# Performance work log

Hardware: AMD Instinct MI355X
Metric: run time of the kernel (lower is better)

The kernel has to match this reference:

```python
import jax, jax.numpy as jnp
import numpy as np

N = 50000
E = 800000
IN_F, HID, OUT_F = 512, 256, 64
BN_EPS = 1e-5


def setup_inputs() -> dict:
    key = jax.random.key(0)
    ks = jax.random.split(key, 8)
    x = jax.random.normal(ks[0], (N, IN_F), dtype=jnp.float32)
    edge_rows = jax.random.randint(ks[1], (E,), 0, N, dtype=jnp.int32)
    edge_cols = jax.random.randint(ks[2], (E,), 0, N, dtype=jnp.int32)
    edge_vals = jax.random.uniform(ks[3], (E,), dtype=jnp.float32)
    # xavier_uniform for weights, zeros for biases (as in the torch module)
    lim1 = float(np.sqrt(6.0 / (IN_F + HID)))
    lim2 = float(np.sqrt(6.0 / (HID + OUT_F)))
    W1 = jax.random.uniform(ks[4], (IN_F, HID), minval=-lim1, maxval=lim1, dtype=jnp.float32)
    b1 = jnp.zeros((HID,), dtype=jnp.float32)
    W2 = jax.random.uniform(ks[5], (HID, OUT_F), minval=-lim2, maxval=lim2, dtype=jnp.float32)
    b2 = jnp.zeros((OUT_F,), dtype=jnp.float32)
    # BatchNorm affine params (torch defaults: weight=1, bias=0)
    gamma1 = jnp.ones((HID,), dtype=jnp.float32)
    beta1 = jnp.zeros((HID,), dtype=jnp.float32)
    gamma2 = jnp.ones((OUT_F,), dtype=jnp.float32)
    beta2 = jnp.zeros((OUT_F,), dtype=jnp.float32)
    return dict(x=x, edge_rows=edge_rows, edge_cols=edge_cols, edge_vals=edge_vals,
                W1=W1, b1=b1, gamma1=gamma1, beta1=beta1,
                W2=W2, b2=b2, gamma2=gamma2, beta2=beta2)


def _spmm(rows, cols, vals, dense):
    # sparse [N,N] @ dense [N,F] via gather + segment-sum scatter
    msgs = vals[:, None] * dense[cols]            # [E, F]
    return jax.ops.segment_sum(msgs, rows, num_segments=N)


def _batchnorm(h, gamma, beta):
    # training-mode BatchNorm1d: batch statistics over nodes (biased var)
    mean = jnp.mean(h, axis=0)
    var = jnp.var(h, axis=0)
    return gamma * (h - mean) * jax.lax.rsqrt(var + BN_EPS) + beta


def reference(x, edge_rows, edge_cols, edge_vals,
              W1, b1, gamma1, beta1, W2, b2, gamma2, beta2):
    # layer 1: GCN conv -> BN -> ReLU (dropout is identity in eval / reference)
    h = _spmm(edge_rows, edge_cols, edge_vals, x @ W1) + b1
    h = jax.nn.relu(_batchnorm(h, gamma1, beta1))
    # layer 2: GCN conv -> BN -> log_softmax over classes
    h = _spmm(edge_rows, edge_cols, edge_vals, h @ W2) + b2
    h = _batchnorm(h, gamma2, beta2)
    return jax.nn.log_softmax(h, axis=1)
```

## Files before the change

### kernel.cpp

```cpp
#include <hip/hip_runtime.h>

typedef __attribute__((ext_vector_type(8))) short short8;
typedef __attribute__((ext_vector_type(4))) float f32x4;
typedef __attribute__((ext_vector_type(8))) unsigned short ushort8;

__device__ __forceinline__ unsigned short f2bf(float f) {
  unsigned int u = __builtin_bit_cast(unsigned int, f);
  u += 0x7fffu + ((u >> 16) & 1u);
  return (unsigned short)(u >> 16);
}
__device__ __forceinline__ float bf2f(unsigned short b) {
  return __builtin_bit_cast(float, ((unsigned int)b) << 16);
}
__device__ __forceinline__ void gload_lds16(const void* g, void* l) {
  __builtin_amdgcn_global_load_lds(
      (const __attribute__((address_space(1))) void*)g,
      (__attribute__((address_space(3))) void*)l, 16, 0, 0);
}

__global__ __launch_bounds__(256) void cvt_w1t(
    const float* __restrict__ W1, unsigned short* __restrict__ W1T)
{
  int idx = blockIdx.x * 256 + threadIdx.x;
  int n = idx >> 9, k = idx & 511;
  W1T[idx] = f2bf(W1[(size_t)k * 256 + n]);
}

__global__ __launch_bounds__(256) void cvt_w2t(
    const float* __restrict__ W2, unsigned short* __restrict__ W2T)
{
  int idx = blockIdx.x * 256 + threadIdx.x;
  int n = idx >> 8, k = idx & 255;
  W2T[idx] = f2bf(W2[(size_t)k * 64 + n]);
}

__global__ __launch_bounds__(256) void gemm1_mfma(
    const float* __restrict__ x,
    const unsigned short* __restrict__ w1t,
    unsigned short* __restrict__ H1,
    int M)
{
  __shared__ unsigned short As[64 * 64];
  __shared__ unsigned short Bs[256 * 64];
  const int tid = threadIdx.x;
  const int wid = tid >> 6, lane = tid & 63;
  const int wc = wid;
  const int m0 = blockIdx.x * 64;

  const int srow = tid >> 3;
  const int ls = ((tid & 7) ^ (srow & 7)) * 8;
  const unsigned short* gB = &w1t[(size_t)srow * 512 + ls];
  char* lB = (char*)Bs + (size_t)wid * 1024;

  f32x4 acc[4][4] = {};

  for (int kt = 0; kt < 8; ++kt) {
    const int k0 = kt * 64;
#pragma unroll
    for (int i = 0; i < 8; ++i)
      gload_lds16(gB + (size_t)i * 32 * 512 + k0, lB + (size_t)i * 4096);
#pragma unroll
    for (int i = 0; i < 2; ++i) {
      int chunk = tid + 256 * i;
      int r = chunk >> 3, c = chunk & 7;
      int grow = m0 + r;
      float v[8] = {0.f, 0.f, 0.f, 0.f, 0.f, 0.f, 0.f, 0.f};
      if (grow < M) {
        float4 lo = *(const float4*)&x[(size_t)grow * 512 + k0 + c * 8];
        float4 hi = *(const float4*)&x[(size_t)grow * 512 + k0 + c * 8 + 4];
        v[0] = lo.x; v[1] = lo.y; v[2] = lo.z; v[3] = lo.w;
        v[4] = hi.x; v[5] = hi.y; v[6] = hi.z; v[7] = hi.w;
      }
      ushort8 o;
#pragma unroll
      for (int j = 0; j < 8; ++j) o[j] = f2bf(v[j]);
      *(ushort8*)((char*)As + r * 128 + ((c ^ (r & 7)) * 16)) = o;
    }
    __syncthreads();

#pragma unroll
    for (int kk = 0; kk < 2; ++kk) {
      short8 a[4], b[4];
#pragma unroll
      for (int m = 0; m < 4; ++m) {
        int row = m * 16 + (lane & 15);
        int phys = (kk * 4 + (lane >> 4)) ^ (row & 7);
        a[m] = *(const short8*)((const char*)As + row * 128 + phys * 16);
      }
#pragma unroll
      for (int n = 0; n < 4; ++n) {
        int col = wc * 64 + n * 16 + (lane & 15);
        int phys = (kk * 4 + (lane >> 4)) ^ (col & 7);
        b[n] = *(const short8*)((const char*)Bs + col * 128 + phys * 16);
      }
#pragma unroll
      for (int m = 0; m < 4; ++m)
#pragma unroll
        for (int n = 0; n < 4; ++n)
          acc[m][n] = __builtin_amdgcn_mfma_f32_16x16x32_bf16(a[m], b[n], acc[m][n], 0, 0, 0);
    }
    __syncthreads();
  }

  const int colbase = wc * 64 + (lane & 15);
#pragma unroll
  for (int m = 0; m < 4; ++m) {
    int rowbase = m0 + m * 16 + (lane >> 4) * 4;
#pragma unroll
    for (int j = 0; j < 4; ++j) {
      int row = rowbase + j;
      if (row < M) {
#pragma unroll
        for (int n = 0; n < 4; ++n)
          H1[(size_t)row * 256 + colbase + n * 16] = f2bf(acc[m][n][j]);
      }
    }
  }
}

__global__ __launch_bounds__(256) void gemm2_mfma(
    const unsigned short* __restrict__ A,
    const unsigned short* __restrict__ w2t,
    const float* __restrict__ scsh,
    unsigned short* __restrict__ H2,
    int M)
{
  __shared__ unsigned short As[128 * 64];
  __shared__ unsigned short Bs[64 * 64];
  const int tid = threadIdx.x;
  const int wid = tid >> 6, lane = tid & 63;
  const int wr = wid >> 1, wc = wid & 1;
  const int m0 = blockIdx.x * 128;

  const int srow = tid >> 3;
  const int ls = ((tid & 7) ^ (srow & 7)) * 8;
  const unsigned short* gB = &w2t[(size_t)srow * 256 + ls];
  char* lB = (char*)Bs + (size_t)wid * 1024;

  f32x4 acc[4][2] = {};

  for (int kt = 0; kt < 4; ++kt) {
    const int k0 = kt * 64;
#pragma unroll
    for (int i = 0; i < 2; ++i)
      gload_lds16(gB + (size_t)i * 32 * 256 + k0, lB + (size_t)i * 4096);
#pragma unroll
    for (int i = 0; i < 4; ++i) {
      int chunk = tid + 256 * i;
      int r = chunk >> 3, c = chunk & 7;
      int gk = k0 + c * 8;
      ushort8 u = *(const ushort8*)&A[(size_t)(m0 + r) * 256 + gk];
      float4 sc0 = *(const float4*)&scsh[gk];
      float4 sc1 = *(const float4*)&scsh[gk + 4];
      float4 sh0 = *(const float4*)&scsh[256 + gk];
      float4 sh1 = *(const float4*)&scsh[256 + gk + 4];
      ushort8 o;
      o[0] = f2bf(fmaxf(bf2f(u[0]) * sc0.x + sh0.x, 0.f));
      o[1] = f2bf(fmaxf(bf2f(u[1]) * sc0.y + sh0.y, 0.f));
      o[2] = f2bf(fmaxf(bf2f(u[2]) * sc0.z + sh0.z, 0.f));
      o[3] = f2bf(fmaxf(bf2f(u[3]) * sc0.w + sh0.w, 0.f));
      o[4] = f2bf(fmaxf(bf2f(u[4]) * sc1.x + sh1.x, 0.f));
      o[5] = f2bf(fmaxf(bf2f(u[5]) * sc1.y + sh1.y, 0.f));
      o[6] = f2bf(fmaxf(bf2f(u[6]) * sc1.z + sh1.z, 0.f));
      o[7] = f2bf(fmaxf(bf2f(u[7]) * sc1.w + sh1.w, 0.f));
      *(ushort8*)((char*)As + r * 128 + ((c ^ (r & 7)) * 16)) = o;
    }
    __syncthreads();

#pragma unroll
    for (int kk = 0; kk < 2; ++kk) {
      short8 a[4], b[2];
#pragma unroll
      for (int m = 0; m < 4; ++m) {
        int row = wr * 64 + m * 16 + (lane & 15);
        int phys = (kk * 4 + (lane >> 4)) ^ (row & 7);
        a[m] = *(const short8*)((const char*)As + row * 128 + phys * 16);
      }
#pragma unroll
      for (int n = 0; n < 2; ++n) {
        int col = wc * 32 + n * 16 + (lane & 15);
        int phys = (kk * 4 + (lane >> 4)) ^ (col & 7);
        b[n] = *(const short8*)((const char*)Bs + col * 128 + phys * 16);
      }
#pragma unroll
      for (int m = 0; m < 4; ++m)
#pragma unroll
        for (int n = 0; n < 2; ++n)
          acc[m][n] = __builtin_amdgcn_mfma_f32_16x16x32_bf16(a[m], b[n], acc[m][n], 0, 0, 0);
    }
    __syncthreads();
  }

  const int colbase = wc * 32 + (lane & 15);
#pragma unroll
  for (int m = 0; m < 4; ++m) {
    int rowbase = m0 + wr * 64 + m * 16 + (lane >> 4) * 4;
#pragma unroll
    for (int j = 0; j < 4; ++j) {
      int row = rowbase + j;
      if (row < M) {
#pragma unroll
        for (int n = 0; n < 2; ++n)
          H2[(size_t)row * 64 + colbase + n * 16] = f2bf(acc[m][n][j]);
      }
    }
  }
}

__global__ __launch_bounds__(256) void edge_hist(
    const int* __restrict__ rows, int* __restrict__ cnt, int E)
{
  int e = blockIdx.x * 256 + threadIdx.x;
  if (e < E) atomicAdd(&cnt[rows[e]], 1);
}

__global__ __launch_bounds__(256) void scan_blocksum(
    const int* __restrict__ cnt, int* __restrict__ bsum, int Nrows)
{
  int i = blockIdx.x * 256 + threadIdx.x;
  int v = (i < Nrows) ? cnt[i] : 0;
#pragma unroll
  for (int off = 1; off < 64; off <<= 1) v += __shfl_xor(v, off);
  __shared__ int wsum[4];
  if ((threadIdx.x & 63) == 0) wsum[threadIdx.x >> 6] = v;
  __syncthreads();
  if (threadIdx.x == 0)
    bsum[blockIdx.x] = wsum[0] + wsum[1] + wsum[2] + wsum[3];
}

__global__ __launch_bounds__(256) void scan_boff(
    const int* __restrict__ bsum, int* __restrict__ boff, int NB)
{
  __shared__ int lds[256];
  int t = threadIdx.x;
  int v = (t < NB) ? bsum[t] : 0;
  lds[t] = v;
  __syncthreads();
  for (int off = 1; off < 256; off <<= 1) {
    int u = (t >= off) ? lds[t - off] : 0;
    __syncthreads();
    lds[t] += u;
    __syncthreads();
  }
  boff[t] = (t == 0) ? 0 : lds[t - 1];
}

__global__ __launch_bounds__(256) void scan_write(
    const int* __restrict__ cnt, const int* __restrict__ boff,
    int* __restrict__ rowptr, int* __restrict__ cursor, int Nrows, int E)
{
  __shared__ int lds[256];
  int t = threadIdx.x;
  int i = blockIdx.x * 256 + t;
  int v = (i < Nrows) ? cnt[i] : 0;
  lds[t] = v;
  __syncthreads();
  for (int off = 1; off < 256; off <<= 1) {
    int u = (t >= off) ? lds[t - off] : 0;
    __syncthreads();
    lds[t] += u;
    __syncthreads();
  }
  int excl = boff[blockIdx.x] + lds[t] - v;
  if (i < Nrows) { rowptr[i] = excl; cursor[i] = excl; }
  if (i == Nrows) rowptr[i] = E;
}

__global__ __launch_bounds__(256) void edge_scatter(
    const int* __restrict__ rows, const int* __restrict__ cols,
    const float* __restrict__ vals, int* __restrict__ cursor,
    int* __restrict__ scols, float* __restrict__ svals, int E)
{
  int e = blockIdx.x * 256 + threadIdx.x;
  if (e < E) {
    int r = rows[e];
    int p = atomicAdd(&cursor[r], 1);
    scols[p] = cols[e];
    svals[p] = vals[e];
  }
}

__global__ __launch_bounds__(256) void spmm_gather_bf(
    const int* __restrict__ rowptr, const int* __restrict__ scols,
    const float* __restrict__ svals, const unsigned short* __restrict__ D,
    unsigned short* __restrict__ out, int Nrows)
{
  const int lane = threadIdx.x & 63;
  const int r = blockIdx.x * 4 + (threadIdx.x >> 6);
  if (r >= Nrows) return;
  const int s = rowptr[r], e = rowptr[r + 1];
  float4 acc = make_float4(0.f, 0.f, 0.f, 0.f);
  int j = s;
  for (; j + 1 < e; j += 2) {
    int c0 = scols[j], c1 = scols[j + 1];
    float v0 = svals[j], v1 = svals[j + 1];
    ushort4 d0 = *(const ushort4*)&D[(size_t)c0 * 256 + lane * 4];
    ushort4 d1 = *(const ushort4*)&D[(size_t)c1 * 256 + lane * 4];
    acc.x = fmaf(v0, bf2f(d0.x), acc.x); acc.y = fmaf(v0, bf2f(d0.y), acc.y);
    acc.z = fmaf(v0, bf2f(d0.z), acc.z); acc.w = fmaf(v0, bf2f(d0.w), acc.w);
    acc.x = fmaf(v1, bf2f(d1.x), acc.x); acc.y = fmaf(v1, bf2f(d1.y), acc.y);
    acc.z = fmaf(v1, bf2f(d1.z), acc.z); acc.w = fmaf(v1, bf2f(d1.w), acc.w);
  }
  if (j < e) {
    int c = scols[j]; float v = svals[j];
    ushort4 d = *(const ushort4*)&D[(size_t)c * 256 + lane * 4];
    acc.x = fmaf(v, bf2f(d.x), acc.x); acc.y = fmaf(v, bf2f(d.y), acc.y);
    acc.z = fmaf(v, bf2f(d.z), acc.z); acc.w = fmaf(v, bf2f(d.w), acc.w);
  }
  ushort4 ov;
  ov.x = f2bf(acc.x); ov.y = f2bf(acc.y); ov.z = f2bf(acc.z); ov.w = f2bf(acc.w);
  *(ushort4*)&out[(size_t)r * 256 + lane * 4] = ov;
}

__global__ __launch_bounds__(256) void spmm_gather_bf64(
    const int* __restrict__ rowptr, const int* __restrict__ scols,
    const float* __restrict__ svals, const unsigned short* __restrict__ D,
    float* __restrict__ out, int Nrows)
{
  const int lane = threadIdx.x & 63;
  const int r = blockIdx.x * 4 + (threadIdx.x >> 6);
  if (r >= Nrows) return;
  const int s = rowptr[r], e = rowptr[r + 1];
  float acc = 0.f;
  int j = s;
  for (; j + 1 < e; j += 2) {
    int c0 = scols[j], c1 = scols[j + 1];
    float v0 = svals[j], v1 = svals[j + 1];
    acc = fmaf(v0, bf2f(D[(size_t)c0 * 64 + lane]), acc);
    acc = fmaf(v1, bf2f(D[(size_t)c1 * 64 + lane]), acc);
  }
  if (j < e) acc = fmaf(svals[j], bf2f(D[(size_t)scols[j] * 64 + lane]), acc);
  out[(size_t)r * 64 + lane] = acc;
}

__global__ __launch_bounds__(256) void bn_stats_bf256(
    const unsigned short* __restrict__ H, float* __restrict__ partials, int Nrows)
{
  const int cc = threadIdx.x & 31;
  const int c = cc * 8;
  const int rr = threadIdx.x >> 5;
  float s[8] = {}, q[8] = {};
  for (int r = blockIdx.x * 8 + rr; r < Nrows; r += gridDim.x * 8) {
    ushort8 u = *(const ushort8*)&H[(size_t)r * 256 + c];
#pragma unroll
    for (int j = 0; j < 8; ++j) {
      float f = bf2f(u[j]);
      s[j] += f; q[j] += f * f;
    }
  }
  __shared__ float lds[256][16];
  float* L = lds[threadIdx.x];
#pragma unroll
  for (int j = 0; j < 8; ++j) { L[j] = s[j]; L[8 + j] = q[j]; }
  __syncthreads();
  if (rr == 0) {
#pragma unroll
    for (int r2 = 1; r2 < 8; ++r2) {
      float* Mm = lds[cc + r2 * 32];
#pragma unroll
      for (int j = 0; j < 8; ++j) { s[j] += Mm[j]; q[j] += Mm[8 + j]; }
    }
    float* P = &partials[(size_t)blockIdx.x * 512];
#pragma unroll
    for (int j = 0; j < 8; ++j) { P[c + j] = s[j]; P[256 + c + j] = q[j]; }
  }
}

__global__ __launch_bounds__(256) void bn_stats64(
    const float* __restrict__ H, float* __restrict__ partials, int Nrows)
{
  const int cc = threadIdx.x % 16;
  const int c = cc * 4;
  const int rr = threadIdx.x / 16;
  float4 s = make_float4(0.f, 0.f, 0.f, 0.f);
  float4 q = make_float4(0.f, 0.f, 0.f, 0.f);
  for (int r = blockIdx.x * 16 + rr; r < Nrows; r += gridDim.x * 16) {
    float4 v = *(const float4*)&H[(size_t)r * 64 + c];
    s.x += v.x; s.y += v.y; s.z += v.z; s.w += v.w;
    q.x += v.x * v.x; q.y += v.y * v.y; q.z += v.z * v.z; q.w += v.w * v.w;
  }
  __shared__ float lds[256][8];
  float* L = lds[threadIdx.x];
  L[0] = s.x; L[1] = s.y; L[2] = s.z; L[3] = s.w;
  L[4] = q.x; L[5] = q.y; L[6] = q.z; L[7] = q.w;
  __syncthreads();
  if (rr == 0) {
#pragma unroll
    for (int r2 = 1; r2 < 16; ++r2) {
      float* Mm = lds[cc + r2 * 16];
      s.x += Mm[0]; s.y += Mm[1]; s.z += Mm[2]; s.w += Mm[3];
      q.x += Mm[4]; q.y += Mm[5]; q.z += Mm[6]; q.w += Mm[7];
    }
    float* P = &partials[(size_t)blockIdx.x * 128];
    *(float4*)&P[c] = s;
    *(float4*)&P[64 + c] = q;
  }
}

template<int C>
__global__ __launch_bounds__(256) void bn_finalize_par(
    const float* __restrict__ partials,
    const float* __restrict__ gamma, const float* __restrict__ beta,
    float* __restrict__ scsh, int G, float invN)
{
  const int c = blockIdx.x;
  const int t = threadIdx.x;
  float sum = 0.f, sq = 0.f;
  for (int g = t; g < G; g += 256) {
    sum += partials[(size_t)g * 2 * C + c];
    sq  += partials[(size_t)g * 2 * C + C + c];
  }
#pragma unroll
  for (int off = 1; off < 64; off <<= 1) {
    sum += __shfl_xor(sum, off);
    sq  += __shfl_xor(sq, off);
  }
  __shared__ float ws[4][2];
  if ((t & 63) == 0) { ws[t >> 6][0] = sum; ws[t >> 6][1] = sq; }
  __syncthreads();
  if (t == 0) {
    sum = ws[0][0] + ws[1][0] + ws[2][0] + ws[3][0];
    sq  = ws[0][1] + ws[1][1] + ws[2][1] + ws[3][1];
    float mean = sum * invN;
    float var = sq * invN - mean * mean;
    float rstd = rsqrtf(var + 1e-5f);
    float sc = gamma[c] * rstd;
    scsh[c] = sc;
    scsh[C + c] = beta[c] - mean * sc;
  }
}

__global__ __launch_bounds__(256) void bn_lsm(
    const float* __restrict__ H, const float* __restrict__ scsh,
    float* __restrict__ out, int Nrows)
{
  int lane = threadIdx.x & 63;
  int r = blockIdx.x * 4 + (threadIdx.x >> 6);
  if (r >= Nrows) return;
  float y = H[(size_t)r * 64 + lane] * scsh[lane] + scsh[64 + lane];
  float m = y;
#pragma unroll
  for (int off = 32; off >= 1; off >>= 1) m = fmaxf(m, __shfl_xor(m, off));
  float ex = expf(y - m);
  float s = ex;
#pragma unroll
  for (int off = 32; off >= 1; off >>= 1) s += __shfl_xor(s, off);
  out[(size_t)r * 64 + lane] = (y - m) - logf(s);
}

extern "C" void kernel_launch(void* const* d_in, const int* in_sizes, int n_in,
                              void* d_out, int out_size, void* d_ws, size_t ws_size,
                              hipStream_t stream) {
  const float* x      = (const float*)d_in[0];
  const int*   erow   = (const int*)  d_in[1];
  const int*   ecol   = (const int*)  d_in[2];
  const float* eval   = (const float*)d_in[3];
  const float* W1     = (const float*)d_in[4];
  const float* gamma1 = (const float*)d_in[6];
  const float* beta1  = (const float*)d_in[7];
  const float* W2     = (const float*)d_in[8];
  const float* gamma2 = (const float*)d_in[10];
  const float* beta2  = (const float*)d_in[11];

  const int N = in_sizes[0] / 512;
  const int E = in_sizes[1];

  char* ws = (char*)d_ws;
  unsigned short* H1b   = (unsigned short*)(ws + 0);
  float* partials1      = (float*)(ws + 0);
  unsigned short* H2b   = (unsigned short*)(ws + 0);
  float* H2AGG          = (float*)(ws + 12800000);
  unsigned short* H1AGGb= (unsigned short*)(ws + 51200000);
  float* partials2      = (float*)(ws + 51200000);
  unsigned short* w1t   = (unsigned short*)(ws + 76865536);
  float* scsh1          = (float*)(ws + 77127680);
  float* scsh2          = (float*)(ws + 77129728);
  int*   rowptr         = (int*)(ws + 77130240);
  int*   cnt            = (int*)(ws + 77330244);
  int*   cursor         = (int*)(ws + 77530244);
  int*   scols          = (int*)(ws + 77730244);
  float* svals          = (float*)(ws + 80930244);
  int*   bsum           = (int*)(ws + 84130244);
  int*   boff           = (int*)(ws + 84131268);
  unsigned short* w2t   = (unsigned short*)(ws + 84132352);

  hipMemsetAsync(cnt, 0, (size_t)N * 4, stream);

  const dim3 blk(256);
  const int eblocks = (E + 255) / 256;
  const int NB = (N + 255) / 256;

  edge_hist<<<eblocks, blk, 0, stream>>>(erow, cnt, E);
  scan_blocksum<<<NB, blk, 0, stream>>>(cnt, bsum, N);
  scan_boff<<<1, blk, 0, stream>>>(bsum, boff, NB);
  scan_write<<<NB + 1, blk, 0, stream>>>(cnt, boff, rowptr, cursor, N, E);
  edge_scatter<<<eblocks, blk, 0, stream>>>(erow, ecol, eval, cursor, scols, svals, E);

  cvt_w1t<<<512, blk, 0, stream>>>(W1, w1t);
  cvt_w2t<<<64, blk, 0, stream>>>(W2, w2t);

  gemm1_mfma<<<(N + 63) / 64, blk, 0, stream>>>(x, w1t, H1b, N);
  spmm_gather_bf<<<(N + 3) / 4, blk, 0, stream>>>(rowptr, scols, svals, H1b, H1AGGb, N);
  bn_stats_bf256<<<256, blk, 0, stream>>>(H1AGGb, partials1, N);
  bn_finalize_par<256><<<256, blk, 0, stream>>>(partials1, gamma1, beta1, scsh1, 256, 1.0f / N);
  gemm2_mfma<<<(N + 127) / 128, blk, 0, stream>>>(H1AGGb, w2t, scsh1, H2b, N);
  spmm_gather_bf64<<<(N + 3) / 4, blk, 0, stream>>>(rowptr, scols, svals, H2b, H2AGG, N);
  bn_stats64<<<256, blk, 0, stream>>>(H2AGG, partials2, N);
  bn_finalize_par<64><<<64, blk, 0, stream>>>(partials2, gamma2, beta2, scsh2, 256, 1.0f / N);
  bn_lsm<<<(N + 3) / 4, blk, 0, stream>>>(H2AGG, scsh2, (float*)d_out, N);
}
```

Measured before the change: 303.9 us.

## Double-buffer GEMM1 tiles, pack CSR col/val pairs, unroll SpMM gathers by four

GEMM1 now uses double-buffered LDS. The next K-tile of x is loaded into registers and W1 is staged into the alternate buffer while MFMAs run on the current tile, so global loads overlap compute. The CSR column indices and values are interleaved into one int2 array, so each edge takes one 8-byte load instead of two separate streams. Both SpMM gather kernels are unrolled by four with two accumulators to raise memory-level parallelism. The cost is twice the LDS in GEMM1, which may lower occupancy, plus a slightly different float summation order.

```diff
diff --git a/kernel.cpp b/kernel.cpp
--- a/kernel.cpp
+++ b/kernel.cpp
@@ -40,8 +40,8 @@
     unsigned short* __restrict__ H1,
     int M)
 {
-  __shared__ unsigned short As[64 * 64];
-  __shared__ unsigned short Bs[256 * 64];
+  __shared__ unsigned short As[2][64 * 64];
+  __shared__ unsigned short Bs[2][256 * 64];
   const int tid = threadIdx.x;
   const int wid = tid >> 6, lane = tid & 63;
   const int wc = wid;
@@ -50,34 +50,55 @@
   const int srow = tid >> 3;
   const int ls = ((tid & 7) ^ (srow & 7)) * 8;
   const unsigned short* gB = &w1t[(size_t)srow * 512 + ls];
-  char* lB = (char*)Bs + (size_t)wid * 1024;
-
-  f32x4 acc[4][4] = {};
-
-  for (int kt = 0; kt < 8; ++kt) {
-    const int k0 = kt * 64;
+
+  const int ar0 = tid >> 3;
+  const int ar1 = ar0 + 32;
+  const int ac  = tid & 7;
+  const int arow0 = m0 + ar0;
+  const int arow1 = m0 + ar1;
+
+  float4 a0lo, a0hi, a1lo, a1hi;
+
+  auto loadA = [&](int k0) {
+    a0lo = make_float4(0.f, 0.f, 0.f, 0.f); a0hi = a0lo; a1lo = a0lo; a1hi = a0lo;
+    if (arow0 < M) {
+      a0lo = *(const float4*)&x[(size_t)arow0 * 512 + k0 + ac * 8];
+      a0hi = *(const float4*)&x[(size_t)arow0 * 512 + k0 + ac * 8 + 4];
+    }
+    if (arow1 < M) {
+      a1lo = *(const float4*)&x[(size_t)arow1 * 512 + k0 + ac * 8];
+      a1hi = *(const float4*)&x[(size_t)arow1 * 512 + k0 + ac * 8 + 4];
+    }
+  };
+  auto writeA = [&](int buf) {
+    float v0[8] = {a0lo.x, a0lo.y, a0lo.z, a0lo.w, a0hi.x, a0hi.y, a0hi.z, a0hi.w};
+    float v1[8] = {a1lo.x, a1lo.y, a1lo.z, a1lo.w, a1hi.x, a1hi.y, a1hi.z, a1hi.w};
+    ushort8 o0, o1;
+#pragma unroll
+    for (int j = 0; j < 8; ++j) { o0[j] = f2bf(v0[j]); o1[j] = f2bf(v1[j]); }
+    *(ushort8*)((char*)As[buf] + ar0 * 128 + ((ac ^ (ar0 & 7)) * 16)) = o0;
+    *(ushort8*)((char*)As[buf] + ar1 * 128 + ((ac ^ (ar1 & 7)) * 16)) = o1;
+  };
+  auto stageB = [&](int k0, int buf) {
+    char* lB = (char*)Bs[buf] + (size_t)wid * 1024;
 #pragma unroll
     for (int i = 0; i < 8; ++i)
       gload_lds16(gB + (size_t)i * 32 * 512 + k0, lB + (size_t)i * 4096);
-#pragma unroll
-    for (int i = 0; i < 2; ++i) {
-      int chunk = tid + 256 * i;
-      int r = chunk >> 3, c = chunk & 7;
-      int grow = m0 + r;
-      float v[8] = {0.f, 0.f, 0.f, 0.f, 0.f, 0.f, 0.f, 0.f};
-      if (grow < M) {
-        float4 lo = *(const float4*)&x[(size_t)grow * 512 + k0 + c * 8];
-        float4 hi = *(const float4*)&x[(size_t)grow * 512 + k0 + c * 8 + 4];
-        v[0] = lo.x; v[1] = lo.y; v[2] = lo.z; v[3] = lo.w;
-        v[4] = hi.x; v[5] = hi.y; v[6] = hi.z; v[7] = hi.w;
-      }
-      ushort8 o;
-#pragma unroll
-      for (int j = 0; j < 8; ++j) o[j] = f2bf(v[j]);
-      *(ushort8*)((char*)As + r * 128 + ((c ^ (r & 7)) * 16)) = o;
-    }
-    __syncthreads();
-
+  };
+
+  f32x4 acc[4][4] = {};
+
+  loadA(0);
+  stageB(0, 0);
+  writeA(0);
+  __syncthreads();
+
+  for (int kt = 0; kt < 8; ++kt) {
+    const int cur = kt & 1, nxt = cur ^ 1;
+    if (kt < 7) {
+      loadA((kt + 1) * 64);
+      stageB((kt + 1) * 64, nxt);
+    }
 #pragma unroll
     for (int kk = 0; kk < 2; ++kk) {
       short8 a[4], b[4];
@@ -85,13 +106,13 @@
       for (int m = 0; m < 4; ++m) {
         int row = m * 16 + (lane & 15);
         int phys = (kk * 4 + (lane >> 4)) ^ (row & 7);
-        a[m] = *(const short8*)((const char*)As + row * 128 + phys * 16);
+        a[m] = *(const short8*)((const char*)As[cur] + row * 128 + phys * 16);
       }
 #pragma unroll
       for (int n = 0; n < 4; ++n) {
         int col = wc * 64 + n * 16 + (lane & 15);
         int phys = (kk * 4 + (lane >> 4)) ^ (col & 7);
-        b[n] = *(const short8*)((const char*)Bs + col * 128 + phys * 16);
+        b[n] = *(const short8*)((const char*)Bs[cur] + col * 128 + phys * 16);
       }
 #pragma unroll
       for (int m = 0; m < 4; ++m)
@@ -99,6 +120,7 @@
         for (int n = 0; n < 4; ++n)
           acc[m][n] = __builtin_amdgcn_mfma_f32_16x16x32_bf16(a[m], b[n], acc[m][n], 0, 0, 0);
     }
+    if (kt < 7) writeA(nxt);
     __syncthreads();
   }
 
@@ -269,68 +291,85 @@
 __global__ __launch_bounds__(256) void edge_scatter(
     const int* __restrict__ rows, const int* __restrict__ cols,
     const float* __restrict__ vals, int* __restrict__ cursor,
-    int* __restrict__ scols, float* __restrict__ svals, int E)
+    int2* __restrict__ spack, int E)
 {
   int e = blockIdx.x * 256 + threadIdx.x;
   if (e < E) {
     int r = rows[e];
     int p = atomicAdd(&cursor[r], 1);
-    scols[p] = cols[e];
-    svals[p] = vals[e];
+    spack[p] = make_int2(cols[e], __float_as_int(vals[e]));
   }
 }
 
 __global__ __launch_bounds__(256) void spmm_gather_bf(
-    const int* __restrict__ rowptr, const int* __restrict__ scols,
-    const float* __restrict__ svals, const unsigned short* __restrict__ D,
+    const int* __restrict__ rowptr, const int2* __restrict__ sp,
+    const unsigned short* __restrict__ D,
     unsigned short* __restrict__ out, int Nrows)
 {
   const int lane = threadIdx.x & 63;
   const int r = blockIdx.x * 4 + (threadIdx.x >> 6);
   if (r >= Nrows) return;
   const int s = rowptr[r], e = rowptr[r + 1];
-  float4 acc = make_float4(0.f, 0.f, 0.f, 0.f);
+  float4 acc0 = make_float4(0.f, 0.f, 0.f, 0.f);
+  float4 acc1 = make_float4(0.f, 0.f, 0.f, 0.f);
   int j = s;
-  for (; j + 1 < e; j += 2) {
-    int c0 = scols[j], c1 = scols[j + 1];
-    float v0 = svals[j], v1 = svals[j + 1];
-    ushort4 d0 = *(const ushort4*)&D[(size_t)c0 * 256 + lane * 4];
-    ushort4 d1 = *(const ushort4*)&D[(size_t)c1 * 256 + lane * 4];
-    acc.x = fmaf(v0, bf2f(d0.x), acc.x); acc.y = fmaf(v0, bf2f(d0.y), acc.y);
-    acc.z = fmaf(v0, bf2f(d0.z), acc.z); acc.w = fmaf(v0, bf2f(d0.w), acc.w);
-    acc.x = fmaf(v1, bf2f(d1.x), acc.x); acc.y = fmaf(v1, bf2f(d1.y), acc.y);
-    acc.z = fmaf(v1, bf2f(d1.z), acc.z); acc.w = fmaf(v1, bf2f(d1.w), acc.w);
-  }
-  if (j < e) {
-    int c = scols[j]; float v = svals[j];
-    ushort4 d = *(const ushort4*)&D[(size_t)c * 256 + lane * 4];
-    acc.x = fmaf(v, bf2f(d.x), acc.x); acc.y = fmaf(v, bf2f(d.y), acc.y);
-    acc.z = fmaf(v, bf2f(d.z), acc.z); acc.w = fmaf(v, bf2f(d.w), acc.w);
+  for (; j + 3 < e; j += 4) {
+    int2 p0 = sp[j], p1 = sp[j + 1], p2 = sp[j + 2], p3 = sp[j + 3];
+    ushort4 d0 = *(const ushort4*)&D[(size_t)p0.x * 256 + lane * 4];
+    ushort4 d1 = *(const ushort4*)&D[(size_t)p1.x * 256 + lane * 4];
+    ushort4 d2 = *(const ushort4*)&D[(size_t)p2.x * 256 + lane * 4];
+    ushort4 d3 = *(const ushort4*)&D[(size_t)p3.x * 256 + lane * 4];
+    float v0 = __int_as_float(p0.y), v1 = __int_as_float(p1.y);
+    float v2 = __int_as_float(p2.y), v3 = __int_as_float(p3.y);
+    acc0.x = fmaf(v0, bf2f(d0.x), acc0.x); acc0.y = fmaf(v0, bf2f(d0.y), acc0.y);
+    acc0.z = fmaf(v0, bf2f(d0.z), acc0.z); acc0.w = fmaf(v0, bf2f(d0.w), acc0.w);
+    acc1.x = fmaf(v1, bf2f(d1.x), acc1.x); acc1.y = fmaf(v1, bf2f(d1.y), acc1.y);
+    acc1.z = fmaf(v1, bf2f(d1.z), acc1.z); acc1.w = fmaf(v1, bf2f(d1.w), acc1.w);
+    acc0.x = fmaf(v2, bf2f(d2.x), acc0.x); acc0.y = fmaf(v2, bf2f(d2.y), acc0.y);
+    acc0.z = fmaf(v2, bf2f(d2.z), acc0.z); acc0.w = fmaf(v2, bf2f(d2.w), acc0.w);
+    acc1.x = fmaf(v3, bf2f(d3.x), acc1.x); acc1.y = fmaf(v3, bf2f(d3.y), acc1.y);
+    acc1.z = fmaf(v3, bf2f(d3.z), acc1.z); acc1.w = fmaf(v3, bf2f(d3.w), acc1.w);
+  }
+  for (; j < e; ++j) {
+    int2 p = sp[j];
+    float v = __int_as_float(p.y);
+    ushort4 d = *(const ushort4*)&D[(size_t)p.x * 256 + lane * 4];
+    acc0.x = fmaf(v, bf2f(d.x), acc0.x); acc0.y = fmaf(v, bf2f(d.y), acc0.y);
+    acc0.z = fmaf(v, bf2f(d.z), acc0.z); acc0.w = fmaf(v, bf2f(d.w), acc0.w);
   }
   ushort4 ov;
-  ov.x = f2bf(acc.x); ov.y = f2bf(acc.y); ov.z = f2bf(acc.z); ov.w = f2bf(acc.w);
+  ov.x = f2bf(acc0.x + acc1.x); ov.y = f2bf(acc0.y + acc1.y);
+  ov.z = f2bf(acc0.z + acc1.z); ov.w = f2bf(acc0.w + acc1.w);
   *(ushort4*)&out[(size_t)r * 256 + lane * 4] = ov;
 }
 
 __global__ __launch_bounds__(256) void spmm_gather_bf64(
-    const int* __restrict__ rowptr, const int* __restrict__ scols,
-    const float* __restrict__ svals, const unsigned short* __restrict__ D,
+    const int* __restrict__ rowptr, const int2* __restrict__ sp,
+    const unsigned short* __restrict__ D,
     float* __restrict__ out, int Nrows)
 {
   const int lane = threadIdx.x & 63;
   const int r = blockIdx.x * 4 + (threadIdx.x >> 6);
   if (r >= Nrows) return;
   const int s = rowptr[r], e = rowptr[r + 1];
-  float acc = 0.f;
+  float acc0 = 0.f, acc1 = 0.f;
   int j = s;
-  for (; j + 1 < e; j += 2) {
-    int c0 = scols[j], c1 = scols[j + 1];
-    float v0 = svals[j], v1 = svals[j + 1];
-    acc = fmaf(v0, bf2f(D[(size_t)c0 * 64 + lane]), acc);
-    acc = fmaf(v1, bf2f(D[(size_t)c1 * 64 + lane]), acc);
-  }
-  if (j < e) acc = fmaf(svals[j], bf2f(D[(size_t)scols[j] * 64 + lane]), acc);
-  out[(size_t)r * 64 + lane] = acc;
+  for (; j + 3 < e; j += 4) {
+    int2 p0 = sp[j], p1 = sp[j + 1], p2 = sp[j + 2], p3 = sp[j + 3];
+    float d0 = bf2f(D[(size_t)p0.x * 64 + lane]);
+    float d1 = bf2f(D[(size_t)p1.x * 64 + lane]);
+    float d2 = bf2f(D[(size_t)p2.x * 64 + lane]);
+    float d3 = bf2f(D[(size_t)p3.x * 64 + lane]);
+    acc0 = fmaf(__int_as_float(p0.y), d0, acc0);
+    acc1 = fmaf(__int_as_float(p1.y), d1, acc1);
+    acc0 = fmaf(__int_as_float(p2.y), d2, acc0);
+    acc1 = fmaf(__int_as_float(p3.y), d3, acc1);
+  }
+  for (; j < e; ++j) {
+    int2 p = sp[j];
+    acc0 = fmaf(__int_as_float(p.y), bf2f(D[(size_t)p.x * 64 + lane]), acc0);
+  }
+  out[(size_t)r * 64 + lane] = acc0 + acc1;
 }
 
 __global__ __launch_bounds__(256) void bn_stats_bf256(
@@ -478,10 +517,9 @@
   int*   rowptr         = (int*)(ws + 77130240);
   int*   cnt            = (int*)(ws + 77330244);
   int*   cursor         = (int*)(ws + 77530244);
-  int*   scols          = (int*)(ws + 77730244);
-  float* svals          = (float*)(ws + 80930244);
-  int*   bsum           = (int*)(ws + 84130244);
-  int*   boff           = (int*)(ws + 84131268);
+  int2*  spack          = (int2*)(ws + 77730248);
+  int*   bsum           = (int*)(ws + 84130248);
+  int*   boff           = (int*)(ws + 84131272);
   unsigned short* w2t   = (unsigned short*)(ws + 84132352);
 
   hipMemsetAsync(cnt, 0, (size_t)N * 4, stream);
@@ -494,17 +532,17 @@
   scan_blocksum<<<NB, blk, 0, stream>>>(cnt, bsum, N);
   scan_boff<<<1, blk, 0, stream>>>(bsum, boff, NB);
   scan_write<<<NB + 1, blk, 0, stream>>>(cnt, boff, rowptr, cursor, N, E);
-  edge_scatter<<<eblocks, blk, 0, stream>>>(erow, ecol, eval, cursor, scols, svals, E);
+  edge_scatter<<<eblocks, blk, 0, stream>>>(erow, ecol, eval, cursor, spack, E);
 
   cvt_w1t<<<512, blk, 0, stream>>>(W1, w1t);
   cvt_w2t<<<64, blk, 0, stream>>>(W2, w2t);
 
   gemm1_mfma<<<(N + 63) / 64, blk, 0, stream>>>(x, w1t, H1b, N);
-  spmm_gather_bf<<<(N + 3) / 4, blk, 0, stream>>>(rowptr, scols, svals, H1b, H1AGGb, N);
+  spmm_gather_bf<<<(N + 3) / 4, blk, 0, stream>>>(rowptr, spack, H1b, H1AGGb, N);
   bn_stats_bf256<<<256, blk, 0, stream>>>(H1AGGb, partials1, N);
   bn_finalize_par<256><<<256, blk, 0, stream>>>(partials1, gamma1, beta1, scsh1, 256, 1.0f / N);
   gemm2_mfma<<<(N + 127) / 128, blk, 0, stream>>>(H1AGGb, w2t, scsh1, H2b, N);
-  spmm_gather_bf64<<<(N + 3) / 4, blk, 0, stream>>>(rowptr, scols, svals, H2b, H2AGG, N);
+  spmm_gather_bf64<<<(N + 3) / 4, blk, 0, stream>>>(rowptr, spack, H2b, H2AGG, N);
   bn_stats64<<<256, blk, 0, stream>>>(H2AGG, partials2, N);
   bn_finalize_par<64><<<64, blk, 0, stream>>>(partials2, gamma2, beta2, scsh2, 256, 1.0f / N);
   bn_lsm<<<(N + 3) / 4, blk, 0, stream>>>(H2AGG, scsh2, (float*)d_out, N);
```

Result: faster. 274.8 us (-9.6%).
